# Kernel optimization log

Hardware: AMD Instinct MI355X
Metric: run time of the kernel (lower is better)

## Reference

```python
import jax, jax.numpy as jnp
import numpy as np

N_NODES = 50000
N_EDGES = 400000
HID = 128
MSG = 128
N_ROUNDS = 2


def setup_inputs() -> dict:
    key = jax.random.key(0)
    ks = jax.random.split(key, 10)
    s = 0.05
    return {
        "x": jax.random.normal(ks[0], (N_NODES, HID), jnp.float32),
        "h": jax.random.normal(ks[1], (N_NODES, HID), jnp.float32),
        "W_msg": jax.random.normal(ks[2], (MSG, 4 * HID), jnp.float32) * s,
        "b_msg": jax.random.normal(ks[3], (MSG,), jnp.float32) * s,
        "w_ih": jax.random.normal(ks[4], (3 * HID, HID + MSG), jnp.float32) * s,
        "w_hh": jax.random.normal(ks[5], (3 * HID, HID), jnp.float32) * s,
        "b_ih": jax.random.normal(ks[6], (3 * HID,), jnp.float32) * s,
        "b_hh": jax.random.normal(ks[7], (3 * HID,), jnp.float32) * s,
        "src": jax.random.randint(ks[8], (N_EDGES,), 0, N_NODES, jnp.int32),
        "dst": jax.random.randint(ks[9], (N_EDGES,), 0, N_NODES, jnp.int32),
    }


def _gru_cell(inp, h, w_ih, w_hh, b_ih, b_hh):
    # torch.nn.GRUCell math
    gi = inp @ w_ih.T + b_ih   # [N, 3H]
    gh = h @ w_hh.T + b_hh     # [N, 3H]
    i_r, i_z, i_n = jnp.split(gi, 3, axis=1)
    h_r, h_z, h_n = jnp.split(gh, 3, axis=1)
    r = jax.nn.sigmoid(i_r + h_r)
    z = jax.nn.sigmoid(i_z + h_z)
    n = jnp.tanh(i_n + r * h_n)
    return (1.0 - z) * n + z * h


def reference(x, h, W_msg, b_msg, w_ih, w_hh, b_ih, b_hh, src, dst):
    n_nodes = x.shape[0]
    ones_e = jnp.ones((src.shape[0], 1), x.dtype)
    for _ in range(N_ROUNDS):
        hd = jax.lax.stop_gradient(h)  # matches h.detach() in message pass
        # edge gather + concat: [E, 4H]
        feat = jnp.concatenate([x[src], hd[src], x[dst], hd[dst]], axis=1)
        m = feat @ W_msg.T + b_msg  # [E, MSG]
        sums = jax.ops.segment_sum(m, dst, num_segments=n_nodes)
        cnt = jax.ops.segment_sum(ones_e, dst, num_segments=n_nodes)
        c = sums / jnp.maximum(cnt, 1.0)  # mean over mailbox; zeros for deg-0
        h = _gru_cell(jnp.concatenate([x, c], axis=1), h, w_ih, w_hh, b_ih, b_hh)
    return h
```

## Files before the change

### kernel.cpp

```cpp
#include <hip/hip_runtime.h>
#include <hip/hip_bf16.h>

typedef __hip_bfloat16 bf16;
typedef __bf16 bf16x8 __attribute__((ext_vector_type(8)));
typedef float  f32x4  __attribute__((ext_vector_type(4)));

#define N_NODES 50000
#define N_EDGES 400000
#define NT 3125
#define HID 128
#define MSG 128


typedef const __attribute__((address_space(1))) unsigned int* as1_u32p;
typedef __attribute__((address_space(3))) unsigned int* as3_u32p;
__device__ __forceinline__ void gll16(const bf16* g, bf16* l) {
    __builtin_amdgcn_global_load_lds((as1_u32p)(const void*)g,
                                     (as3_u32p)(void*)l, 16, 0, 0);
}

__global__ __launch_bounds__(256)
void gemm_sd_kernel(const bf16* __restrict__ XT,
                    const bf16* __restrict__ HT,
                    const bf16* __restrict__ W,
                    bf16* __restrict__ O, int M) {
    constexpr int K = 256, J = 256;
    __shared__ __align__(16) bf16 Ws[64 * K];

    const int bid = blockIdx.x;
    const int mt  = (bid >> 5) * 8 + (bid & 7);
    const int bnt = (bid >> 3) & 3;
    if (mt * 256 >= M) return;
    const int bm = mt * 256;
    const int bn = bnt * 64;
    const int tid = threadIdx.x;

    const bf16* wsrc = W + (size_t)bnt * 16384;
    #pragma unroll
    for (int i = 0; i < 8; ++i)
        gll16(wsrc + i * 2048 + tid * 8, &Ws[i * 2048 + tid * 8]);
    __syncthreads();

    const int w    = tid >> 6;
    const int lane = tid & 63;
    const int lr   = lane & 15;
    const int kg   = lane >> 4;
    const int mbase = bm + w * 64;

    int tile[4];
    #pragma unroll
    for (int fm = 0; fm < 4; ++fm) {
        int t = (mbase + fm * 16) >> 4;
        tile[fm] = (t < NT) ? t : NT - 1;
    }

    f32x4 acc[4][4] = {};

    #pragma unroll
    for (int k0 = 0; k0 < K; k0 += 32) {
        bf16x8 a[4];
        #pragma unroll
        for (int fm = 0; fm < 4; ++fm) {
            const bf16* ap = (k0 < 128)
                ? XT + ((size_t)tile[fm] * 32 + (k0 >> 3) + kg) * 128 + lr * 8
                : HT + ((size_t)tile[fm] * 16 + ((k0 - 128) >> 3) + kg) * 128 + lr * 8;
            a[fm] = *reinterpret_cast<const bf16x8*>(ap);
        }
        const int kcb = (k0 >> 3) + kg;
        #pragma unroll
        for (int fn = 0; fn < 4; ++fn) {
            bf16x8 b = *reinterpret_cast<const bf16x8*>(
                &Ws[(kcb * 64 + ((fn * 16 + lr) ^ (kcb & 7))) * 8]);
            #pragma unroll
            for (int fm = 0; fm < 4; ++fm)
                acc[fm][fn] = __builtin_amdgcn_mfma_f32_16x16x32_bf16(
                    a[fm], b, acc[fm][fn], 0, 0, 0);
        }
    }

    __syncthreads();
    #pragma unroll
    for (int fn = 0; fn < 4; ++fn) {
        int col = fn * 16 + lr;
        #pragma unroll
        for (int fm = 0; fm < 4; ++fm) {
            int rbase = w * 64 + fm * 16 + kg * 4;
            #pragma unroll
            for (int r = 0; r < 4; ++r) {
                int row = rbase + r;
                int cs = ((((col >> 3) ^ ((row >> 2) & 7))) << 3) | (col & 7);
                Ws[row * 64 + cs] = __float2bfloat16(acc[fm][fn][r]);
            }
        }
    }
    __syncthreads();
    const int colblk = tid & 7;
    const int rbase_o = tid >> 3;
    #pragma unroll
    for (int it = 0; it < 8; ++it) {
        int row = it * 32 + rbase_o;
        int grow = bm + row;
        if (grow < M) {
            int g = (row >> 2) & 7;
            const float4 v = *reinterpret_cast<const float4*>(
                &Ws[row * 64 + ((colblk ^ g) << 3)]);
            *reinterpret_cast<float4*>(O + (size_t)grow * J + bn + colblk * 8) = v;
        }
    }
}

__device__ __forceinline__ float fast_sigmoid(float x) {
    return 1.0f / (1.0f + __expf(-x));
}
__device__ __forceinline__ float fast_tanh(float x) {
    float e = __expf(-2.0f * fabsf(x));
    float t = (1.0f - e) / (1.0f + e);
    return copysignf(t, x);
}

template <int FINAL>
__global__ __launch_bounds__(256, 4)
void gates_kernel(const bf16* __restrict__ XT,
                  const bf16* __restrict__ HT,
                  const bf16* __restrict__ Wg,
                  const float* __restrict__ bg,
                  const float* __restrict__ h0,
                  float* __restrict__ h_out,
                  bf16* __restrict__ HTout,
                  int M) {
    const int bid = blockIdx.x;
    const int mt  = (bid >> 6) * 8 + (bid & 7);
    const int q   = (bid >> 3) & 7;
    if (mt * 256 >= M) return;

    const int tid  = threadIdx.x;
    const int w    = tid >> 6;
    const int lane = tid & 63;
    const int lr   = lane & 15;
    const int kg   = lane >> 4;
    const int mbase = mt * 256 + w * 64;

    int tile[4];
    #pragma unroll
    for (int fm = 0; fm < 4; ++fm) {
        int t = (mbase + fm * 16) >> 4;
        tile[fm] = (t < NT) ? t : NT - 1;
    }
    const bf16* Wb = Wg + ((size_t)kg * 512 + q * 64 + lr) * 8;

    f32x4 acc[4][4] = {};

    #pragma unroll
    for (int ch = 0; ch < 12; ++ch) {
        bf16x8 a[4];
        #pragma unroll
        for (int fm = 0; fm < 4; ++fm) {
            const bf16* ap = (ch < 8)
                ? XT + ((size_t)tile[fm] * 32 + ch * 4 + kg) * 128 + lr * 8
                : HT + ((size_t)tile[fm] * 16 + (ch - 8) * 4 + kg) * 128 + lr * 8;
            a[fm] = *reinterpret_cast<const bf16x8*>(ap);
        }
        #pragma unroll
        for (int gi = 0; gi < 3; ++gi) {
            const int g = (ch < 8) ? gi : ((gi == 2) ? 3 : gi);
            bf16x8 b = *reinterpret_cast<const bf16x8*>(
                Wb + ((size_t)ch * 4 * 512 + g * 16) * 8);
            #pragma unroll
            for (int fm = 0; fm < 4; ++fm)
                acc[fm][g] = __builtin_amdgcn_mfma_f32_16x16x32_bf16(
                    a[fm], b, acc[fm][g], 0, 0, 0);
        }
    }

    const float br  = bg[q * 64 + lr];
    const float bz  = bg[q * 64 + 16 + lr];
    const float bin = bg[q * 64 + 32 + lr];
    const float bhn = bg[q * 64 + 48 + lr];
    const int c = q * 16 + lr;
    #pragma unroll
    for (int fm = 0; fm < 4; ++fm) {
        #pragma unroll
        for (int r = 0; r < 4; ++r) {
            const int row = mbase + fm * 16 + kg * 4 + r;
            if (row >= M) continue;
            float rr = fast_sigmoid(acc[fm][0][r] + br);
            float zz = fast_sigmoid(acc[fm][1][r] + bz);
            float nn = fast_tanh(acc[fm][2][r] + bin +
                                 rr * (acc[fm][3][r] + bhn));
            const size_t hti = ((size_t)(row >> 4) * 16 + (c >> 3)) * 128
                               + (row & 15) * 8 + (c & 7);
            float hin;
            if (FINAL) {
                hin = __bfloat162float(HT[hti]);
            } else {
                hin = h0[(size_t)row * 128 + c];
            }
            float hv = (1.0f - zz) * nn + zz * hin;
            if (FINAL) {
                h_out[(size_t)row * 128 + c] = hv;
            } else {
                HTout[hti] = __float2bfloat16(hv);
            }
        }
    }
}

#define WSD_N  65536
#define WG_N   196608
__global__ __launch_bounds__(256)
void prep_weights_kernel(const float* __restrict__ W_msg,
                         const float* __restrict__ w_ih,
                         const float* __restrict__ w_hh,
                         const float* __restrict__ b_ih,
                         const float* __restrict__ b_hh,
                         bf16* __restrict__ Wsd,
                         bf16* __restrict__ Wg,
                         float* __restrict__ bg) {
    int gid = blockIdx.x * 256 + threadIdx.x;
    if (gid < WSD_N) {
        int bn_t = gid >> 14;
        int r    = gid & 16383;
        int kc   = r >> 9;
        int r2   = r & 511;
        int js   = r2 >> 3;
        int e    = r2 & 7;
        int jj   = bn_t * 64 + (js ^ (kc & 7));
        int k    = kc * 8 + e;
        float v = (jj < 128) ? W_msg[jj * 512 + k]
                             : W_msg[(jj - 128) * 512 + 256 + k];
        Wsd[gid] = __float2bfloat16(v);
    } else if (gid < WSD_N + WG_N) {
        int i  = gid - WSD_N;
        int kc = i >> 12;
        int j  = (i >> 3) & 511;
        int e  = i & 7;
        int k  = kc * 8 + e;
        int q = j >> 6, g = (j >> 4) & 3, lr = j & 15;
        int c = q * 16 + lr;
        float v;
        if (k < 256) v = (g < 3) ? w_ih[(size_t)(g * 128 + c) * 256 + k] : 0.0f;
        else         v = (g == 2) ? 0.0f
                       : w_hh[(size_t)(((g == 3) ? 2 : g) * 128 + c) * 128 + (k - 256)];
        Wg[i] = __float2bfloat16(v);
    } else if (gid < WSD_N + WG_N + 512) {
        int jp = gid - WSD_N - WG_N;
        int q = jp >> 6, g = (jp >> 4) & 3, lr = jp & 15;
        int c = q * 16 + lr;
        float v;
        if (g == 0)      v = b_ih[c] + b_hh[c];
        else if (g == 1) v = b_ih[128 + c] + b_hh[128 + c];
        else if (g == 2) v = b_ih[256 + c];
        else             v = b_hh[256 + c];
        bg[jp] = v;
    }
}

__global__ __launch_bounds__(256)
void conv_xa_kernel(const float* __restrict__ x, const float* __restrict__ h0,
                    bf16* __restrict__ XT, bf16* __restrict__ HT0, int N) {
    int gid = blockIdx.x * 256 + threadIdx.x;
    if (gid >= N * 32) return;
    const int half = (gid >= N * 16);
    const int i  = half ? gid - N * 16 : gid;
    const int v  = i >> 4;
    const int kc = i & 15;
    const float* src = (half ? h0 : x) + (size_t)v * 128 + kc * 8;
    const float4 f0 = *reinterpret_cast<const float4*>(src);
    const float4 f1 = *reinterpret_cast<const float4*>(src + 4);
    bf16 tmp[8];
    tmp[0] = __float2bfloat16(f0.x); tmp[1] = __float2bfloat16(f0.y);
    tmp[2] = __float2bfloat16(f0.z); tmp[3] = __float2bfloat16(f0.w);
    tmp[4] = __float2bfloat16(f1.x); tmp[5] = __float2bfloat16(f1.y);
    tmp[6] = __float2bfloat16(f1.z); tmp[7] = __float2bfloat16(f1.w);
    bf16* dst = half
        ? HT0 + ((size_t)(v >> 4) * 16 + kc) * 128 + (v & 15) * 8
        : XT  + ((size_t)(v >> 4) * 32 + kc) * 128 + (v & 15) * 8;
    *reinterpret_cast<float4*>(dst) = *reinterpret_cast<const float4*>(tmp);
}

__global__ __launch_bounds__(256)
void deg_kernel(const int* __restrict__ dst, int* __restrict__ cnt, int E) {
    int e = blockIdx.x * 256 + threadIdx.x;
    if (e < E) atomicAdd(&cnt[dst[e]], 1);
}

__global__ __launch_bounds__(256)
void csr_alloc_kernel(const int* __restrict__ cnt, int* __restrict__ off,
                      int* __restrict__ total, int N) {
    int v = blockIdx.x * 256 + threadIdx.x;
    int lane = threadIdx.x & 63;
    int c = (v < N) ? cnt[v] : 0;
    int s = c;
    #pragma unroll
    for (int d = 1; d < 64; d <<= 1) {
        int t = __shfl_up(s, d, 64);
        if (lane >= d) s += t;
    }
    int wave_total = __shfl(s, 63, 64);
    int base = 0;
    if (lane == 63) base = atomicAdd(total, wave_total);
    base = __shfl(base, 63, 64);
    if (v < N) off[v] = base + s - c;
}

__global__ __launch_bounds__(256)
void fill_csr_kernel(const int* __restrict__ src, const int* __restrict__ dst,
                     const int* __restrict__ off, int* __restrict__ cursor,
                     int* __restrict__ csr, int E) {
    int e = blockIdx.x * 256 + threadIdx.x;
    if (e >= E) return;
    int d = dst[e];
    int pos = atomicAdd(&cursor[d], 1);
    csr[off[d] + pos] = src[e];
}

__global__ __launch_bounds__(256)
void agg_kernel(const bf16* __restrict__ SD, const int* __restrict__ csr,
                const int* __restrict__ off, const int* __restrict__ cnt,
                const float* __restrict__ b_msg, bf16* __restrict__ XT, int N) {
    const int v    = (blockIdx.x * 256 + threadIdx.x) >> 6;
    const int lane = threadIdx.x & 63;
    if (v >= N) return;
    const int deg  = cnt[v];
    const int base = off[v];

    float ax[4] = {0.f, 0.f, 0.f, 0.f};
    float ay[4] = {0.f, 0.f, 0.f, 0.f};
    int k = 0;
    for (; k + 3 < deg; k += 4) {
        #pragma unroll
        for (int u = 0; u < 4; ++u) {
            int s0 = csr[base + k + u];
            unsigned q = *reinterpret_cast<const unsigned*>(
                SD + (size_t)s0 * 256 + lane * 2);
            ax[u] += __uint_as_float(q << 16);
            ay[u] += __uint_as_float(q & 0xffff0000u);
        }
    }
    for (; k < deg; ++k) {
        int s0 = csr[base + k];
        unsigned q = *reinterpret_cast<const unsigned*>(
            SD + (size_t)s0 * 256 + lane * 2);
        ax[0] += __uint_as_float(q << 16);
        ay[0] += __uint_as_float(q & 0xffff0000u);
    }

    float ox = 0.f, oy = 0.f;
    if (deg > 0) {
        unsigned ud = *reinterpret_cast<const unsigned*>(
            SD + (size_t)v * 256 + 128 + lane * 2);
        float inv = 1.0f / (float)deg;
        const float2 bm = *reinterpret_cast<const float2*>(b_msg + lane * 2);
        ox = ((ax[0] + ax[1]) + (ax[2] + ax[3])) * inv + __uint_as_float(ud << 16)         + bm.x;
        oy = ((ay[0] + ay[1]) + (ay[2] + ay[3])) * inv + __uint_as_float(ud & 0xffff0000u) + bm.y;
    }
    __hip_bfloat162 o2;
    o2.x = __float2bfloat16(ox);
    o2.y = __float2bfloat16(oy);
    const size_t ci = ((size_t)(v >> 4) * 32 + 16 + (lane >> 2)) * 128
                      + (v & 15) * 8 + ((lane * 2) & 7);
    *reinterpret_cast<__hip_bfloat162*>(XT + ci) = o2;
}

extern "C" void kernel_launch(void* const* d_in, const int* in_sizes, int n_in,
                              void* d_out, int out_size, void* d_ws, size_t ws_size,
                              hipStream_t stream) {
    const float* x     = (const float*)d_in[0];
    const float* h0    = (const float*)d_in[1];
    const float* W_msg = (const float*)d_in[2];
    const float* b_msg = (const float*)d_in[3];
    const float* w_ih  = (const float*)d_in[4];
    const float* w_hh  = (const float*)d_in[5];
    const float* b_ih  = (const float*)d_in[6];
    const float* b_hh  = (const float*)d_in[7];
    const int*   src   = (const int*)d_in[8];
    const int*   dst   = (const int*)d_in[9];
    float* h = (float*)d_out;

    char* ws = (char*)d_ws;
    size_t off_b = 0;
    auto alloc = [&](size_t bytes) -> void* {
        void* p = ws + off_b;
        off_b = (off_b + bytes + 255) & ~(size_t)255;
        return p;
    };
    int*   meta   = (int*)  alloc(((size_t)2 * N_NODES + 64) * 4);
    int*   cnt    = meta;
    int*   cursor = meta + N_NODES;
    int*   total  = meta + 2 * N_NODES;
    int*   off    = (int*)  alloc((size_t)N_NODES * 4);
    int*   csr    = (int*)  alloc((size_t)N_EDGES * 4);
    bf16*  Wsd_b  = (bf16*) alloc((size_t)WSD_N * 2);
    bf16*  Wg_b   = (bf16*) alloc((size_t)WG_N * 2);
    float* bg     = (float*)alloc(512 * 4);
    bf16*  XT     = (bf16*) alloc((size_t)NT * 32 * 128 * 2);
    bf16*  HT0    = (bf16*) alloc((size_t)NT * 16 * 128 * 2);
    bf16*  HT1    = (bf16*) alloc((size_t)NT * 16 * 128 * 2);
    bf16*  SD     = (bf16*) alloc((size_t)N_NODES * 256 * 2);

    hipMemsetAsync(meta, 0, ((size_t)2 * N_NODES + 64) * 4, stream);
    deg_kernel<<<(N_EDGES + 255) / 256, 256, 0, stream>>>(dst, cnt, N_EDGES);
    csr_alloc_kernel<<<(N_NODES + 255) / 256, 256, 0, stream>>>(cnt, off, total, N_NODES);
    fill_csr_kernel<<<(N_EDGES + 255) / 256, 256, 0, stream>>>(src, dst, off, cursor,
                                                               csr, N_EDGES);
    prep_weights_kernel<<<(WSD_N + WG_N + 512 + 255) / 256, 256, 0, stream>>>(
        W_msg, w_ih, w_hh, b_ih, b_hh, Wsd_b, Wg_b, bg);
    conv_xa_kernel<<<(N_NODES * 32 + 255) / 256, 256, 0, stream>>>(
        x, h0, XT, HT0, N_NODES);

    const int SD_GRID    = 25 * 32;
    const int GATES_GRID = 25 * 64;

    gemm_sd_kernel<<<SD_GRID, 256, 0, stream>>>(XT, HT0, Wsd_b, SD, N_NODES);
    agg_kernel<<<(N_NODES * 64 + 255) / 256, 256, 0, stream>>>(
        SD, csr, off, cnt, b_msg, XT, N_NODES);
    gates_kernel<0><<<GATES_GRID, 256, 0, stream>>>(
        XT, HT0, Wg_b, bg, h0, nullptr, HT1, N_NODES);

    gemm_sd_kernel<<<SD_GRID, 256, 0, stream>>>(XT, HT1, Wsd_b, SD, N_NODES);
    agg_kernel<<<(N_NODES * 64 + 255) / 256, 256, 0, stream>>>(
        SD, csr, off, cnt, b_msg, XT, N_NODES);
    gates_kernel<1><<<GATES_GRID, 256, 0, stream>>>(
        XT, HT1, Wg_b, bg, nullptr, h, nullptr, N_NODES);
}
```

Baseline: 229.5 us.

## Fold destination-side message projection into GRU input weights

The message GEMM now computes only the source-side projection (128 columns instead of 256), and the destination term W_d·[x;h] plus b_msg is algebraically folded into the GRU input weights via a composed weight computed in a new prep kernel. Zero-degree nodes get a correction term computed directly in the aggregation kernel so the mean stays zero. This halves the message GEMM work and the per-node gather buffer size, but the gates GEMM's h-chunk loop now runs four gate groups and is no longer fully unrolled. The gates kernel also reads h from the bf16 tiled copy instead of fp32 h0 in the first round, which adds precision risk.

```diff
diff --git a/kernel.cpp b/kernel.cpp
--- a/kernel.cpp
+++ b/kernel.cpp
@@ -23,16 +23,15 @@
 void gemm_sd_kernel(const bf16* __restrict__ XT,
                     const bf16* __restrict__ HT,
                     const bf16* __restrict__ W,
-                    bf16* __restrict__ O, int M) {
-    constexpr int K = 256, J = 256;
+                    bf16* __restrict__ Sb, int M) {
+    constexpr int K = 256;
     __shared__ __align__(16) bf16 Ws[64 * K];
 
     const int bid = blockIdx.x;
-    const int mt  = (bid >> 5) * 8 + (bid & 7);
-    const int bnt = (bid >> 3) & 3;
+    const int mt  = (bid >> 4) * 8 + (bid & 7);
+    const int bnt = (bid >> 3) & 1;
     if (mt * 256 >= M) return;
     const int bm = mt * 256;
-    const int bn = bnt * 64;
     const int tid = threadIdx.x;
 
     const bf16* wsrc = W + (size_t)bnt * 16384;
@@ -104,7 +103,8 @@
             int g = (row >> 2) & 7;
             const float4 v = *reinterpret_cast<const float4*>(
                 &Ws[row * 64 + ((colblk ^ g) << 3)]);
-            *reinterpret_cast<float4*>(O + (size_t)grow * J + bn + colblk * 8) = v;
+            *reinterpret_cast<float4*>(Sb + (size_t)grow * 128 + bnt * 64
+                                       + colblk * 8) = v;
         }
     }
 }
@@ -124,7 +124,6 @@
                   const bf16* __restrict__ HT,
                   const bf16* __restrict__ Wg,
                   const float* __restrict__ bg,
-                  const float* __restrict__ h0,
                   float* __restrict__ h_out,
                   bf16* __restrict__ HTout,
                   int M) {
@@ -160,9 +159,8 @@
                 : HT + ((size_t)tile[fm] * 16 + (ch - 8) * 4 + kg) * 128 + lr * 8;
             a[fm] = *reinterpret_cast<const bf16x8*>(ap);
         }
-        #pragma unroll
-        for (int gi = 0; gi < 3; ++gi) {
-            const int g = (ch < 8) ? gi : ((gi == 2) ? 3 : gi);
+        const int ng = (ch < 8) ? 3 : 4;
+        for (int g = 0; g < ng; ++g) {
             bf16x8 b = *reinterpret_cast<const bf16x8*>(
                 Wb + ((size_t)ch * 4 * 512 + g * 16) * 8);
             #pragma unroll
@@ -189,12 +187,7 @@
                                  rr * (acc[fm][3][r] + bhn));
             const size_t hti = ((size_t)(row >> 4) * 16 + (c >> 3)) * 128
                                + (row & 15) * 8 + (c & 7);
-            float hin;
-            if (FINAL) {
-                hin = __bfloat162float(HT[hti]);
-            } else {
-                hin = h0[(size_t)row * 128 + c];
-            }
+            float hin = __bfloat162float(HT[hti]);
             float hv = (1.0f - zz) * nn + zz * hin;
             if (FINAL) {
                 h_out[(size_t)row * 128 + c] = hv;
@@ -205,53 +198,79 @@
     }
 }
 
-#define WSD_N  65536
-#define WG_N   196608
-__global__ __launch_bounds__(256)
-void prep_weights_kernel(const float* __restrict__ W_msg,
-                         const float* __restrict__ w_ih,
+#define WS_N 32768
+__global__ __launch_bounds__(256)
+void prep_small_kernel(const float* __restrict__ W_msg,
+                       bf16* __restrict__ Ws, float* __restrict__ Wd_f,
+                       float* __restrict__ WdT) {
+    int gid = blockIdx.x * 256 + threadIdx.x;
+    if (gid < WS_N) {
+        int bnt = gid >> 14;
+        int r   = gid & 16383;
+        int kc  = r >> 9;
+        int r2  = r & 511;
+        int js  = r2 >> 3;
+        int e   = r2 & 7;
+        int jj  = bnt * 64 + (js ^ (kc & 7));
+        int k   = kc * 8 + e;
+        Ws[gid] = __float2bfloat16(W_msg[(size_t)jj * 512 + k]);
+    } else if (gid < WS_N + 32768) {
+        int i = gid - WS_N;
+        int cc = i >> 8, k = i & 255;
+        Wd_f[i] = W_msg[(size_t)cc * 512 + 256 + k];
+    } else if (gid < WS_N + 65536) {
+        int i = gid - WS_N - 32768;
+        int k = i >> 7, cc = i & 127;
+        WdT[i] = W_msg[(size_t)cc * 512 + 256 + k];
+    }
+}
+
+__global__ __launch_bounds__(256)
+void prep_compose_kernel(const float* __restrict__ w_ih,
                          const float* __restrict__ w_hh,
                          const float* __restrict__ b_ih,
                          const float* __restrict__ b_hh,
-                         bf16* __restrict__ Wsd,
-                         bf16* __restrict__ Wg,
-                         float* __restrict__ bg) {
-    int gid = blockIdx.x * 256 + threadIdx.x;
-    if (gid < WSD_N) {
-        int bn_t = gid >> 14;
-        int r    = gid & 16383;
-        int kc   = r >> 9;
-        int r2   = r & 511;
-        int js   = r2 >> 3;
-        int e    = r2 & 7;
-        int jj   = bn_t * 64 + (js ^ (kc & 7));
-        int k    = kc * 8 + e;
-        float v = (jj < 128) ? W_msg[jj * 512 + k]
-                             : W_msg[(jj - 128) * 512 + 256 + k];
-        Wsd[gid] = __float2bfloat16(v);
-    } else if (gid < WSD_N + WG_N) {
-        int i  = gid - WSD_N;
-        int kc = i >> 12;
-        int j  = (i >> 3) & 511;
-        int e  = i & 7;
-        int k  = kc * 8 + e;
-        int q = j >> 6, g = (j >> 4) & 3, lr = j & 15;
-        int c = q * 16 + lr;
-        float v;
-        if (k < 256) v = (g < 3) ? w_ih[(size_t)(g * 128 + c) * 256 + k] : 0.0f;
-        else         v = (g == 2) ? 0.0f
-                       : w_hh[(size_t)(((g == 3) ? 2 : g) * 128 + c) * 128 + (k - 256)];
-        Wg[i] = __float2bfloat16(v);
-    } else if (gid < WSD_N + WG_N + 512) {
-        int jp = gid - WSD_N - WG_N;
-        int q = jp >> 6, g = (jp >> 4) & 3, lr = jp & 15;
-        int c = q * 16 + lr;
-        float v;
-        if (g == 0)      v = b_ih[c] + b_hh[c];
-        else if (g == 1) v = b_ih[128 + c] + b_hh[128 + c];
-        else if (g == 2) v = b_ih[256 + c];
-        else             v = b_hh[256 + c];
-        bg[jp] = v;
+                         const float* __restrict__ b_msg,
+                         const float* __restrict__ WdT,
+                         bf16* __restrict__ Wg, float* __restrict__ bg) {
+    __shared__ float WcL[128];
+    const int j = blockIdx.x;
+    const int q = j >> 6, g = (j >> 4) & 3, lr = j & 15;
+    const int c = q * 16 + lr;
+    const int t = threadIdx.x;
+    if (t < 128)
+        WcL[t] = (g < 3) ? w_ih[(size_t)(g * 128 + c) * 256 + 128 + t] : 0.0f;
+    __syncthreads();
+
+    float comp = 0.0f;
+    const float* wrow = WdT + (size_t)t * 128;
+    #pragma unroll 4
+    for (int cc = 0; cc < 128; ++cc) comp += WcL[cc] * wrow[cc];
+
+    float base;
+    int k;
+    if (t < 128) {
+        k = t;
+        base = (g < 3) ? w_ih[(size_t)(g * 128 + c) * 256 + t] : 0.0f;
+        int kc2 = (128 + t) >> 3, e2 = (128 + t) & 7;
+        Wg[((size_t)kc2 * 512 + j) * 8 + e2] = __float2bfloat16(WcL[t]);
+    } else {
+        int kh = t - 128;
+        k = 256 + kh;
+        base = (g == 2) ? 0.0f
+             : w_hh[(size_t)(((g == 3) ? 2 : g) * 128 + c) * 128 + kh];
+    }
+    int kc = k >> 3, e = k & 7;
+    Wg[((size_t)kc * 512 + j) * 8 + e] = __float2bfloat16(base + comp);
+
+    if (t == 0) {
+        float s;
+        if (g == 0)      s = b_ih[c] + b_hh[c];
+        else if (g == 1) s = b_ih[128 + c] + b_hh[128 + c];
+        else if (g == 2) s = b_ih[256 + c];
+        else             s = b_hh[256 + c];
+        for (int cc = 0; cc < 128; ++cc) s += WcL[cc] * b_msg[cc];
+        bg[j] = s;
     }
 }
 
@@ -315,45 +334,61 @@
 }
 
 __global__ __launch_bounds__(256)
-void agg_kernel(const bf16* __restrict__ SD, const int* __restrict__ csr,
+void agg_kernel(const bf16* __restrict__ Sb, const int* __restrict__ csr,
                 const int* __restrict__ off, const int* __restrict__ cnt,
-                const float* __restrict__ b_msg, bf16* __restrict__ XT, int N) {
+                const float* __restrict__ b_msg, const float* __restrict__ Wd,
+                const bf16* __restrict__ HT, bf16* __restrict__ XT, int N) {
     const int v    = (blockIdx.x * 256 + threadIdx.x) >> 6;
     const int lane = threadIdx.x & 63;
     if (v >= N) return;
     const int deg  = cnt[v];
-    const int base = off[v];
-
-    float ax[4] = {0.f, 0.f, 0.f, 0.f};
-    float ay[4] = {0.f, 0.f, 0.f, 0.f};
-    int k = 0;
-    for (; k + 3 < deg; k += 4) {
-        #pragma unroll
-        for (int u = 0; u < 4; ++u) {
-            int s0 = csr[base + k + u];
-            unsigned q = *reinterpret_cast<const unsigned*>(
-                SD + (size_t)s0 * 256 + lane * 2);
-            ax[u] += __uint_as_float(q << 16);
-            ay[u] += __uint_as_float(q & 0xffff0000u);
-        }
-    }
-    for (; k < deg; ++k) {
-        int s0 = csr[base + k];
-        unsigned q = *reinterpret_cast<const unsigned*>(
-            SD + (size_t)s0 * 256 + lane * 2);
-        ax[0] += __uint_as_float(q << 16);
-        ay[0] += __uint_as_float(q & 0xffff0000u);
-    }
-
-    float ox = 0.f, oy = 0.f;
+    float ox, oy;
+
     if (deg > 0) {
-        unsigned ud = *reinterpret_cast<const unsigned*>(
-            SD + (size_t)v * 256 + 128 + lane * 2);
+        const int base = off[v];
+        float ax[4] = {0.f, 0.f, 0.f, 0.f};
+        float ay[4] = {0.f, 0.f, 0.f, 0.f};
+        int k = 0;
+        for (; k + 3 < deg; k += 4) {
+            #pragma unroll
+            for (int u = 0; u < 4; ++u) {
+                int s0 = csr[base + k + u];
+                unsigned qv = *reinterpret_cast<const unsigned*>(
+                    Sb + (size_t)s0 * 128 + lane * 2);
+                ax[u] += __uint_as_float(qv << 16);
+                ay[u] += __uint_as_float(qv & 0xffff0000u);
+            }
+        }
+        for (; k < deg; ++k) {
+            int s0 = csr[base + k];
+            unsigned qv = *reinterpret_cast<const unsigned*>(
+                Sb + (size_t)s0 * 128 + lane * 2);
+            ax[0] += __uint_as_float(qv << 16);
+            ay[0] += __uint_as_float(qv & 0xffff0000u);
+        }
         float inv = 1.0f / (float)deg;
-        const float2 bm = *reinterpret_cast<const float2*>(b_msg + lane * 2);
-        ox = ((ax[0] + ax[1]) + (ax[2] + ax[3])) * inv + __uint_as_float(ud << 16)         + bm.x;
-        oy = ((ay[0] + ay[1]) + (ay[2] + ay[3])) * inv + __uint_as_float(ud & 0xffff0000u) + bm.y;
-    }
+        ox = ((ax[0] + ax[1]) + (ax[2] + ax[3])) * inv;
+        oy = ((ay[0] + ay[1]) + (ay[2] + ay[3])) * inv;
+    } else {
+        const int c0 = lane * 2;
+        ox = -b_msg[c0];
+        oy = -b_msg[c0 + 1];
+        const int tt = v >> 4, rr = v & 15;
+        for (int kc = 0; kc < 32; ++kc) {
+            const bf16* ap = (kc < 16)
+                ? XT + ((size_t)tt * 32 + kc) * 128 + rr * 8
+                : HT + ((size_t)tt * 16 + (kc - 16)) * 128 + rr * 8;
+            bf16x8 a8 = *reinterpret_cast<const bf16x8*>(ap);
+            #pragma unroll
+            for (int e = 0; e < 8; ++e) {
+                float av = (float)a8[e];
+                int k = kc * 8 + e;
+                ox -= av * Wd[(size_t)c0 * 256 + k];
+                oy -= av * Wd[(size_t)(c0 + 1) * 256 + k];
+            }
+        }
+    }
+
     __hip_bfloat162 o2;
     o2.x = __float2bfloat16(ox);
     o2.y = __float2bfloat16(oy);
@@ -390,36 +425,41 @@
     int*   total  = meta + 2 * N_NODES;
     int*   off    = (int*)  alloc((size_t)N_NODES * 4);
     int*   csr    = (int*)  alloc((size_t)N_EDGES * 4);
-    bf16*  Wsd_b  = (bf16*) alloc((size_t)WSD_N * 2);
-    bf16*  Wg_b   = (bf16*) alloc((size_t)WG_N * 2);
+    bf16*  Ws_b   = (bf16*) alloc((size_t)WS_N * 2);
+    float* Wd_f   = (float*)alloc((size_t)32768 * 4);
+    float* WdT_f  = (float*)alloc((size_t)32768 * 4);
+    bf16*  Wg_b   = (bf16*) alloc((size_t)48 * 512 * 8 * 2);
     float* bg     = (float*)alloc(512 * 4);
     bf16*  XT     = (bf16*) alloc((size_t)NT * 32 * 128 * 2);
     bf16*  HT0    = (bf16*) alloc((size_t)NT * 16 * 128 * 2);
     bf16*  HT1    = (bf16*) alloc((size_t)NT * 16 * 128 * 2);
-    bf16*  SD     = (bf16*) alloc((size_t)N_NODES * 256 * 2);
+    bf16*  Sb     = (bf16*) alloc((size_t)N_NODES * 128 * 2);
 
     hipMemsetAsync(meta, 0, ((size_t)2 * N_NODES + 64) * 4, stream);
     deg_kernel<<<(N_EDGES + 255) / 256, 256, 0, stream>>>(dst, cnt, N_EDGES);
     csr_alloc_kernel<<<(N_NODES + 255) / 256, 256, 0, stream>>>(cnt, off, total, N_NODES);
     fill_csr_kernel<<<(N_EDGES + 255) / 256, 256, 0, stream>>>(src, dst, off, cursor,
                                                                csr, N_EDGES);
-    prep_weights_kernel<<<(WSD_N + WG_N + 512 + 255) / 256, 256, 0, stream>>>(
-        W_msg, w_ih, w_hh, b_ih, b_hh, Wsd_b, Wg_b, bg);
+    prep_small_kernel<<<(WS_N + 65536 + 255) / 256, 256, 0, stream>>>(
+        W_msg, Ws_b, Wd_f, WdT_f);
+    prep_compose_kernel<<<512, 256, 0, stream>>>(
+        w_ih, w_hh, b_ih, b_hh, b_msg, WdT_f, Wg_b, bg);
     conv_xa_kernel<<<(N_NODES * 32 + 255) / 256, 256, 0, stream>>>(
         x, h0, XT, HT0, N_NODES);
 
-    const int SD_GRID    = 25 * 32;
+    const int SD_GRID    = 25 * 16;
     const int GATES_GRID = 25 * 64;
-
-    gemm_sd_kernel<<<SD_GRID, 256, 0, stream>>>(XT, HT0, Wsd_b, SD, N_NODES);
-    agg_kernel<<<(N_NODES * 64 + 255) / 256, 256, 0, stream>>>(
-        SD, csr, off, cnt, b_msg, XT, N_NODES);
+    const int AGG_GRID   = (N_NODES * 64 + 255) / 256;
+
+    gemm_sd_kernel<<<SD_GRID, 256, 0, stream>>>(XT, HT0, Ws_b, Sb, N_NODES);
+    agg_kernel<<<AGG_GRID, 256, 0, stream>>>(
+        Sb, csr, off, cnt, b_msg, Wd_f, HT0, XT, N_NODES);
     gates_kernel<0><<<GATES_GRID, 256, 0, stream>>>(
-        XT, HT0, Wg_b, bg, h0, nullptr, HT1, N_NODES);
-
-    gemm_sd_kernel<<<SD_GRID, 256, 0, stream>>>(XT, HT1, Wsd_b, SD, N_NODES);
-    agg_kernel<<<(N_NODES * 64 + 255) / 256, 256, 0, stream>>>(
-        SD, csr, off, cnt, b_msg, XT, N_NODES);
+        XT, HT0, Wg_b, bg, nullptr, HT1, N_NODES);
+
+    gemm_sd_kernel<<<SD_GRID, 256, 0, stream>>>(XT, HT1, Ws_b, Sb, N_NODES);
+    agg_kernel<<<AGG_GRID, 256, 0, stream>>>(
+        Sb, csr, off, cnt, b_msg, Wd_f, HT1, XT, N_NODES);
     gates_kernel<1><<<GATES_GRID, 256, 0, stream>>>(
-        XT, HT1, Wg_b, bg, nullptr, h, nullptr, N_NODES);
-}
+        XT, HT1, Wg_b, bg, h, nullptr, N_NODES);
+}
```

Measured after the change: 250.0 us. 1.09x slower.
